# Kernel optimization log

Measured on AMD Instinct MI355X. Metric: run time of the kernel, lower is better.

## Reference

```python
import jax, jax.numpy as jnp
import numpy as np

B, L, C, D, K = 32, 36864, 16, 512, 24


def setup_inputs() -> dict:
    key = jax.random.key(0)
    ks = jax.random.split(key, 5)
    x = jax.random.normal(ks[0], (B, L, C), jnp.float32)
    # offset-conv weights scaled small so predicted offsets are O(0.2) (kaiming-ish but tame)
    w_off = jax.random.normal(ks[1], (2 * K, C, K), jnp.float32) * 0.01
    b_off = jax.random.normal(ks[2], (2 * K,), jnp.float32) * 0.05
    w_def = jax.random.normal(ks[3], (D, C, K), jnp.float32) * (2.0 / (C * K)) ** 0.5
    b_def = jax.random.normal(ks[4], (D,), jnp.float32) * 0.05
    return {"x": x, "w_off": w_off, "b_off": b_off, "w_def": w_def, "b_def": b_def}


def reference(x, w_off, b_off, w_def, b_def):
    # x: [B, L, C] -> torch view [B, C, 1, L]; H == 1 throughout.
    Bn, Ln, Cn = x.shape
    twoK, _, Kn = w_off.shape
    Lout = Ln // Kn
    xc = jnp.transpose(x, (0, 2, 1))                 # [B, C, L]
    xk = xc.reshape(Bn, Cn, Lout, Kn)                # stride == kernel -> non-overlapping windows
    # offset conv: [B, 2K, Lout]
    off = jnp.einsum('bclk,ock->bol', xk, w_off) + b_off[None, :, None]
    off = off.reshape(Bn, Kn, 2, Lout)               # channel 2k -> dy, 2k+1 -> dx (torchvision layout)
    dy = jnp.transpose(off[:, :, 0, :], (0, 2, 1))   # [B, Lout, K]
    dx = jnp.transpose(off[:, :, 1, :], (0, 2, 1))   # [B, Lout, K]
    # sampling positions along width; base = w_out*K + k
    base = jnp.arange(Lout * Kn, dtype=x.dtype).reshape(Lout, Kn)
    px = base[None] + dx                             # [B, Lout, K]
    # height bilinear weight: with H=1, contribution at h=0 is max(0, 1-|dy|)
    wy = jnp.maximum(jnp.array(0, x.dtype), 1.0 - jnp.abs(dy))
    # width bilinear with zero padding (torchvision bilinear_interpolate semantics)
    valid = (px > -1.0) & (px < Ln)
    x0 = jnp.floor(px)
    lw = px - x0                                     # weight for right neighbor
    i0 = x0.astype(jnp.int32)
    i1 = i0 + 1
    m0 = (valid & (i0 >= 0) & (i0 < Ln)).astype(x.dtype)
    m1 = (valid & (i1 >= 0) & (i1 < Ln)).astype(x.dtype)
    i0c = jnp.broadcast_to(jnp.clip(i0, 0, Ln - 1).reshape(Bn, 1, Lout * Kn), (Bn, Cn, Lout * Kn))
    i1c = jnp.broadcast_to(jnp.clip(i1, 0, Ln - 1).reshape(Bn, 1, Lout * Kn), (Bn, Cn, Lout * Kn))
    v0 = jnp.take_along_axis(xc, i0c, axis=2).reshape(Bn, Cn, Lout, Kn)
    v1 = jnp.take_along_axis(xc, i1c, axis=2).reshape(Bn, Cn, Lout, Kn)
    val = (v0 * ((1.0 - lw) * m0)[:, None] + v1 * (lw * m1)[:, None]) * wy[:, None]  # [B,C,Lout,K]
    out = jnp.einsum('bclk,dck->bld', val, w_def) + b_def  # [B, Lout, D]
    return out
```

## Files before the change

kernel.cpp:

```cpp
#include <hip/hip_runtime.h>
#include <stdint.h>

#define BATCH 32
#define LLEN  36864
#define CCH   16
#define DOUT  512
#define KW    24
#define LOUT  1536
#define MROWS (BATCH * LOUT)
#define CK    384
#define TWOK  48

typedef float fx4 __attribute__((ext_vector_type(4)));
typedef float f32x4 __attribute__((ext_vector_type(4)));
typedef __bf16 bf16x8 __attribute__((ext_vector_type(8)));
typedef uint32_t u32x4 __attribute__((ext_vector_type(4)));

__device__ __forceinline__ void gload16(void* lds, const void* g)
{
    __builtin_amdgcn_global_load_lds(
        (const __attribute__((address_space(1))) uint32_t*)g,
        (__attribute__((address_space(3))) uint32_t*)lds, 16, 0, 0);
}

__global__ __launch_bounds__(256) void prep_kernel(
    const float* __restrict__ w_off, const float* __restrict__ w_def,
    __bf16* __restrict__ woff_b, __bf16* __restrict__ wdef_b)
{
    int idx = blockIdx.x * 256 + threadIdx.x;
    if (idx < TWOK * CK) {
        int o = idx / CK, rem = idx % CK;
        int k = rem >> 4, c = rem & 15;
        woff_b[idx] = (__bf16)w_off[o * CK + c * KW + k];
    }
    if (idx < DOUT * CK) {
        int d = idx / CK, rem = idx % CK;
        int k = rem >> 4, c = rem & 15;
        wdef_b[idx] = (__bf16)w_def[d * CK + c * KW + k];
    }
}

#define BM 96
#define BN 512
#define BK 64

__global__ __launch_bounds__(512) void gemm_fused(
    const float* __restrict__ x, const __bf16* __restrict__ woff_b,
    const float* __restrict__ b_off, const __bf16* __restrict__ Bw,
    const float* __restrict__ bias, float* __restrict__ out)
{
    __shared__ __bf16 As[BM * BK];
    __shared__ char  smemB[BN * BK * 2];
    __bf16* Bs    = (__bf16*)smemB;
    __bf16* WoffS = (__bf16*)smemB;
    float*  offS  = (float*)(smemB + 38144);

    const int t = threadIdx.x;
    const int m0 = blockIdx.x * BM;
    const int wave = t >> 6, lane = t & 63;
    const int quad = lane >> 4, l16 = lane & 15;
    const int wr = wave >> 2, wc = wave & 3;

    const int mloc = t >> 2, k4 = t & 3;
    const int Mrow = m0 + mloc;
    const int b    = m0 / LOUT;
    const int lb   = Mrow - b * LOUT;
    const float* xb = x + (size_t)b * LLEN * CCH;

#pragma unroll
    for (int i = 0; i < 5; ++i) {
        int q = t + 512 * i;
        if (q < 2304) {
            int row = q / 48, cc = q - row * 48;
            *(u32x4*)&WoffS[row * 392 + cc * 8] =
                *(const u32x4*)&woff_b[row * CK + cc * 8];
        }
    }
    __syncthreads();

    if (wave < 6) {
        const float* xr = x + (size_t)(m0 + wave * 16 + l16) * CK;
        f32x4 oacc[3] = {};
#pragma unroll
        for (int ks = 0; ks < 12; ++ks) {
            int k0 = ks * 32 + quad * 8;
            fx4 a0 = *(const fx4*)&xr[k0];
            fx4 a1 = *(const fx4*)&xr[k0 + 4];
            bf16x8 af;
            af[0] = (__bf16)a0.x; af[1] = (__bf16)a0.y;
            af[2] = (__bf16)a0.z; af[3] = (__bf16)a0.w;
            af[4] = (__bf16)a1.x; af[5] = (__bf16)a1.y;
            af[6] = (__bf16)a1.z; af[7] = (__bf16)a1.w;
#pragma unroll
            for (int j = 0; j < 3; ++j) {
                bf16x8 bf = *(const bf16x8*)&WoffS[(j * 16 + l16) * 392 + k0];
                oacc[j] = __builtin_amdgcn_mfma_f32_16x16x32_bf16(af, bf, oacc[j], 0, 0, 0);
            }
        }
        float bo[3];
#pragma unroll
        for (int j = 0; j < 3; ++j) bo[j] = b_off[j * 16 + l16];
#pragma unroll
        for (int j = 0; j < 3; ++j)
#pragma unroll
            for (int r = 0; r < 4; ++r)
                offS[(wave * 16 + quad * 4 + r) * 49 + j * 16 + l16] = oacc[j][r] + bo[j];
    }
    __syncthreads();

    uint32_t dxyr[6];
    if (t < 4 * BM) {
#pragma unroll
        for (int cc = 0; cc < 6; ++cc) {
            int kk = 4 * cc + k4;
            float dy = offS[mloc * 49 + 2 * kk];
            float dx = offS[mloc * 49 + 2 * kk + 1];
            union { __bf16 h[2]; uint32_t u; } p;
            p.h[0] = (__bf16)dy; p.h[1] = (__bf16)dx;
            dxyr[cc] = p.u;
        }
    }

    f32x4 acc[3][8] = {};
    fx4 g0[4], g1[4];
    float w0, w1;

    auto load_pair = [&](uint32_t pk, int kk) {
        union { uint32_t u; __bf16 h[2]; } p; p.u = pk;
        float dy = (float)p.h[0], dx = (float)p.h[1];
        float wy  = fmaxf(0.f, 1.f - fabsf(dy));
        float px  = (float)(lb * KW + kk) + dx;
        float x0f = floorf(px);
        float lw  = px - x0f;
        int   i0  = (int)x0f;
        bool valid = (px > -1.0f) && (px < (float)LLEN);
        w0 = (valid && i0 >= 0)         ? (1.f - lw) * wy : 0.f;
        w1 = (valid && (i0 + 1) < LLEN) ? lw * wy         : 0.f;
        int i0c = min(max(i0, 0), LLEN - 1);
        int i1c = min(max(i0 + 1, 0), LLEN - 1);
        const fx4* p0 = (const fx4*)&xb[(size_t)i0c * CCH];
        const fx4* p1 = (const fx4*)&xb[(size_t)i1c * CCH];
#pragma unroll
        for (int q = 0; q < 4; ++q) { g0[q] = p0[q]; g1[q] = p1[q]; }
    };

    if (t < 4 * BM) load_pair(dxyr[0], k4);

#pragma unroll
    for (int cc = 0; cc < 6; ++cc) {
        const int kt = cc * BK;
        __syncthreads();
        if (t < 4 * BM) {
            bf16x8 oa, ob;
#pragma unroll
            for (int q = 0; q < 2; ++q) {
                fx4 v0 = g0[q], v1 = g1[q];
                oa[q * 4 + 0] = (__bf16)(w0 * v0.x + w1 * v1.x);
                oa[q * 4 + 1] = (__bf16)(w0 * v0.y + w1 * v1.y);
                oa[q * 4 + 2] = (__bf16)(w0 * v0.z + w1 * v1.z);
                oa[q * 4 + 3] = (__bf16)(w0 * v0.w + w1 * v1.w);
            }
#pragma unroll
            for (int q = 0; q < 2; ++q) {
                fx4 v0 = g0[q + 2], v1 = g1[q + 2];
                ob[q * 4 + 0] = (__bf16)(w0 * v0.x + w1 * v1.x);
                ob[q * 4 + 1] = (__bf16)(w0 * v0.y + w1 * v1.y);
                ob[q * 4 + 2] = (__bf16)(w0 * v0.z + w1 * v1.z);
                ob[q * 4 + 3] = (__bf16)(w0 * v0.w + w1 * v1.w);
            }
            int g = 2 * k4;
            *(bf16x8*)&As[mloc * BK + ((g ^ (mloc & 7)) * 8)]       = oa;
            *(bf16x8*)&As[mloc * BK + (((g + 1) ^ (mloc & 7)) * 8)] = ob;
        }
#pragma unroll
        for (int it = 0; it < 8; ++it) {
            int q = it * 512 + t;
            int r = q >> 3, c8 = q & 7;
            int sc = c8 ^ (r & 7);
            gload16(&Bs[q * 8], Bw + (size_t)r * CK + kt + sc * 8);
        }
        __syncthreads();
        if (cc + 1 < 6 && t < 4 * BM)
            load_pair(dxyr[cc + 1], 4 * (cc + 1) + k4);
#pragma unroll
        for (int ks = 0; ks < 2; ++ks) {
            bf16x8 af[3], bfr[8];
#pragma unroll
            for (int i = 0; i < 3; ++i) {
                int row = wr * 48 + i * 16 + l16;
                af[i] = *(const bf16x8*)&As[row * BK + (((ks * 4 + quad) ^ (row & 7)) * 8)];
            }
#pragma unroll
            for (int j = 0; j < 8; ++j) {
                int col = wc * 128 + j * 16 + l16;
                bfr[j] = *(const bf16x8*)&Bs[col * BK + (((ks * 4 + quad) ^ (col & 7)) * 8)];
            }
#pragma unroll
            for (int i = 0; i < 3; ++i)
#pragma unroll
                for (int j = 0; j < 8; ++j)
                    acc[i][j] = __builtin_amdgcn_mfma_f32_16x16x32_bf16(
                        af[i], bfr[j], acc[i][j], 0, 0, 0);
        }
    }

#pragma unroll
    for (int j = 0; j < 8; ++j) {
        int col = wc * 128 + j * 16 + l16;
        float bj = bias[col];
#pragma unroll
        for (int i = 0; i < 3; ++i) {
            int rowb = m0 + wr * 48 + i * 16 + quad * 4;
#pragma unroll
            for (int r = 0; r < 4; ++r)
                out[(size_t)(rowb + r) * DOUT + col] = acc[i][j][r] + bj;
        }
    }
}

extern "C" void kernel_launch(void* const* d_in, const int* in_sizes, int n_in,
                              void* d_out, int out_size, void* d_ws, size_t ws_size,
                              hipStream_t stream)
{
    const float* x     = (const float*)d_in[0];
    const float* w_off = (const float*)d_in[1];
    const float* b_off = (const float*)d_in[2];
    const float* w_def = (const float*)d_in[3];
    const float* b_def = (const float*)d_in[4];
    float* out = (float*)d_out;

    char* ws = (char*)d_ws;
    __bf16* wdef_b = (__bf16*)ws;
    __bf16* woff_b = (__bf16*)(ws + 393216);

    prep_kernel<<<768, 256, 0, stream>>>(w_off, w_def, woff_b, wdef_b);
    gemm_fused<<<MROWS / BM, 512, 0, stream>>>(x, woff_b, b_off, wdef_b, b_def, out);
}
```

Measured before the change: 196.2 us.

## Read weight fragments directly from global memory and double-buffer A tile in LDS

The B (w_def) tile is no longer staged through LDS. Each wave now loads its bf16 fragments straight from global/L2. The A tile is double-buffered, which removes one of the two barriers per K-step, and s_setprio is raised around the MFMA section. This is meant to cut LDS traffic, LDS footprint and synchronisation, at the cost of many more redundant global loads of the weights, served by cache. Each of the 4 wave-rows reads the same weights, so L2/L1 bandwidth and latency may become the bottleneck.

```diff
diff --git a/kernel.cpp b/kernel.cpp
--- a/kernel.cpp
+++ b/kernel.cpp
@@ -16,13 +16,6 @@
 typedef __bf16 bf16x8 __attribute__((ext_vector_type(8)));
 typedef uint32_t u32x4 __attribute__((ext_vector_type(4)));
 
-__device__ __forceinline__ void gload16(void* lds, const void* g)
-{
-    __builtin_amdgcn_global_load_lds(
-        (const __attribute__((address_space(1))) uint32_t*)g,
-        (__attribute__((address_space(3))) uint32_t*)lds, 16, 0, 0);
-}
-
 __global__ __launch_bounds__(256) void prep_kernel(
     const float* __restrict__ w_off, const float* __restrict__ w_def,
     __bf16* __restrict__ woff_b, __bf16* __restrict__ wdef_b)
@@ -49,11 +42,10 @@
     const float* __restrict__ b_off, const __bf16* __restrict__ Bw,
     const float* __restrict__ bias, float* __restrict__ out)
 {
-    __shared__ __bf16 As[BM * BK];
-    __shared__ char  smemB[BN * BK * 2];
-    __bf16* Bs    = (__bf16*)smemB;
-    __bf16* WoffS = (__bf16*)smemB;
-    float*  offS  = (float*)(smemB + 38144);
+    __shared__ char smem[57344];
+    __bf16* WoffS = (__bf16*)smem;
+    float*  offS  = (float*)(smem + 38144);
+    __bf16* As    = (__bf16*)smem;
 
     const int t = threadIdx.x;
     const int m0 = blockIdx.x * BM;
@@ -149,7 +141,7 @@
 #pragma unroll
     for (int cc = 0; cc < 6; ++cc) {
         const int kt = cc * BK;
-        __syncthreads();
+        __bf16* Ab = As + (cc & 1) * (BM * BK);
         if (t < 4 * BM) {
             bf16x8 oa, ob;
 #pragma unroll
@@ -169,31 +161,25 @@
                 ob[q * 4 + 3] = (__bf16)(w0 * v0.w + w1 * v1.w);
             }
             int g = 2 * k4;
-            *(bf16x8*)&As[mloc * BK + ((g ^ (mloc & 7)) * 8)]       = oa;
-            *(bf16x8*)&As[mloc * BK + (((g + 1) ^ (mloc & 7)) * 8)] = ob;
-        }
-#pragma unroll
-        for (int it = 0; it < 8; ++it) {
-            int q = it * 512 + t;
-            int r = q >> 3, c8 = q & 7;
-            int sc = c8 ^ (r & 7);
-            gload16(&Bs[q * 8], Bw + (size_t)r * CK + kt + sc * 8);
+            *(bf16x8*)&Ab[mloc * BK + ((g ^ (mloc & 7)) * 8)]       = oa;
+            *(bf16x8*)&Ab[mloc * BK + (((g + 1) ^ (mloc & 7)) * 8)] = ob;
         }
         __syncthreads();
         if (cc + 1 < 6 && t < 4 * BM)
             load_pair(dxyr[cc + 1], 4 * (cc + 1) + k4);
+        __builtin_amdgcn_s_setprio(1);
 #pragma unroll
         for (int ks = 0; ks < 2; ++ks) {
             bf16x8 af[3], bfr[8];
 #pragma unroll
             for (int i = 0; i < 3; ++i) {
                 int row = wr * 48 + i * 16 + l16;
-                af[i] = *(const bf16x8*)&As[row * BK + (((ks * 4 + quad) ^ (row & 7)) * 8)];
+                af[i] = *(const bf16x8*)&Ab[row * BK + (((ks * 4 + quad) ^ (row & 7)) * 8)];
             }
 #pragma unroll
             for (int j = 0; j < 8; ++j) {
                 int col = wc * 128 + j * 16 + l16;
-                bfr[j] = *(const bf16x8*)&Bs[col * BK + (((ks * 4 + quad) ^ (col & 7)) * 8)];
+                bfr[j] = *(const bf16x8*)&Bw[(size_t)col * CK + kt + (ks * 4 + quad) * 8];
             }
 #pragma unroll
             for (int i = 0; i < 3; ++i)
@@ -202,6 +188,7 @@
                     acc[i][j] = __builtin_amdgcn_mfma_f32_16x16x32_bf16(
                         af[i], bfr[j], acc[i][j], 0, 0, 0);
         }
+        __builtin_amdgcn_s_setprio(0);
     }
 
 #pragma unroll
```

After: 227.4 us. 15.9% more time.

## Double-buffer weight tiles in half-K phases with manual waitcnt pipelining

Applied to the files above, without the earlier changes.

Splits each 64-wide K step into two 32-wide phases and uses two LDS buffers for the weight tile. The DMA for the next phase is issued while MFMAs run on the current one, with explicit vmcnt/lgkmcnt waits, raw s_barriers, sched barriers and priority bumps around the MFMA blocks. The goal is to hide global-to-LDS load latency that the old single-buffer loop exposed behind its two __syncthreads per step. The risk is that the hand-counted vmcnt values (which differ between waves depending on how many gather loads are in flight) could be wrong, and LDS use grows to 76KB.

```diff
diff --git a/kernel.cpp b/kernel.cpp
--- a/kernel.cpp
+++ b/kernel.cpp
@@ -16,6 +16,11 @@
 typedef __bf16 bf16x8 __attribute__((ext_vector_type(8)));
 typedef uint32_t u32x4 __attribute__((ext_vector_type(4)));
 
+#define VMCNT(n)  asm volatile("s_waitcnt vmcnt(" #n ")" ::: "memory")
+#define LGKMCNT0  asm volatile("s_waitcnt lgkmcnt(0)" ::: "memory")
+#define SCHEDB    __builtin_amdgcn_sched_barrier(0)
+#define SBAR      __builtin_amdgcn_s_barrier()
+
 __device__ __forceinline__ void gload16(void* lds, const void* g)
 {
     __builtin_amdgcn_global_load_lds(
@@ -49,11 +54,12 @@
     const float* __restrict__ b_off, const __bf16* __restrict__ Bw,
     const float* __restrict__ bias, float* __restrict__ out)
 {
-    __shared__ __bf16 As[BM * BK];
-    __shared__ char  smemB[BN * BK * 2];
-    __bf16* Bs    = (__bf16*)smemB;
-    __bf16* WoffS = (__bf16*)smemB;
-    float*  offS  = (float*)(smemB + 38144);
+    __shared__ char smem[77824];
+    __bf16* As  = (__bf16*)smem;
+    __bf16* Bs0 = (__bf16*)(smem + 12288);
+    __bf16* Bs1 = (__bf16*)(smem + 45056);
+    __bf16* WoffS = (__bf16*)smem;
+    float*  offS  = (float*)(smem + 45056);
 
     const int t = threadIdx.x;
     const int m0 = blockIdx.x * BM;
@@ -144,12 +150,47 @@
         for (int q = 0; q < 4; ++q) { g0[q] = p0[q]; g1[q] = p1[q]; }
     };
 
+    auto dma_phase = [&](int ph, __bf16* buf) {
+#pragma unroll
+        for (int it = 0; it < 4; ++it) {
+            int q = it * 512 + t;
+            int c = q >> 2, s = q & 3;
+            int ss = s ^ ((c >> 1) & 3);
+            gload16(&buf[q * 8], Bw + (size_t)c * CK + ph * 32 + ss * 8);
+        }
+    };
+
+    auto mfma_phase = [&](int ks, const __bf16* Bsb) {
+        bf16x8 af[3], bfr[8];
+#pragma unroll
+        for (int i = 0; i < 3; ++i) {
+            int row = wr * 48 + i * 16 + l16;
+            af[i] = *(const bf16x8*)&As[row * BK + (((ks * 4 + quad) ^ (row & 7)) * 8)];
+        }
+#pragma unroll
+        for (int j = 0; j < 8; ++j) {
+            int col = wc * 128 + j * 16 + l16;
+            bfr[j] = *(const bf16x8*)&Bsb[col * 32 + ((quad ^ ((col >> 1) & 3)) * 8)];
+        }
+#pragma unroll
+        for (int i = 0; i < 3; ++i)
+#pragma unroll
+            for (int j = 0; j < 8; ++j)
+                acc[i][j] = __builtin_amdgcn_mfma_f32_16x16x32_bf16(
+                    af[i], bfr[j], acc[i][j], 0, 0, 0);
+    };
+
     if (t < 4 * BM) load_pair(dxyr[0], k4);
+    SCHEDB;
+    dma_phase(0, Bs0);
+    SCHEDB;
 
 #pragma unroll
     for (int cc = 0; cc < 6; ++cc) {
-        const int kt = cc * BK;
-        __syncthreads();
+        SBAR;
+        SCHEDB;
+        VMCNT(4);
+        SCHEDB;
         if (t < 4 * BM) {
             bf16x8 oa, ob;
 #pragma unroll
@@ -172,36 +213,36 @@
             *(bf16x8*)&As[mloc * BK + ((g ^ (mloc & 7)) * 8)]       = oa;
             *(bf16x8*)&As[mloc * BK + (((g + 1) ^ (mloc & 7)) * 8)] = ob;
         }
-#pragma unroll
-        for (int it = 0; it < 8; ++it) {
-            int q = it * 512 + t;
-            int r = q >> 3, c8 = q & 7;
-            int sc = c8 ^ (r & 7);
-            gload16(&Bs[q * 8], Bw + (size_t)r * CK + kt + sc * 8);
-        }
-        __syncthreads();
+        SCHEDB;
+        dma_phase(2 * cc + 1, Bs1);
+        SCHEDB;
         if (cc + 1 < 6 && t < 4 * BM)
             load_pair(dxyr[cc + 1], 4 * (cc + 1) + k4);
-#pragma unroll
-        for (int ks = 0; ks < 2; ++ks) {
-            bf16x8 af[3], bfr[8];
-#pragma unroll
-            for (int i = 0; i < 3; ++i) {
-                int row = wr * 48 + i * 16 + l16;
-                af[i] = *(const bf16x8*)&As[row * BK + (((ks * 4 + quad) ^ (row & 7)) * 8)];
-            }
-#pragma unroll
-            for (int j = 0; j < 8; ++j) {
-                int col = wc * 128 + j * 16 + l16;
-                bfr[j] = *(const bf16x8*)&Bs[col * BK + (((ks * 4 + quad) ^ (col & 7)) * 8)];
-            }
-#pragma unroll
-            for (int i = 0; i < 3; ++i)
-#pragma unroll
-                for (int j = 0; j < 8; ++j)
-                    acc[i][j] = __builtin_amdgcn_mfma_f32_16x16x32_bf16(
-                        af[i], bfr[j], acc[i][j], 0, 0, 0);
-        }
+        SCHEDB;
+        LGKMCNT0;
+        SCHEDB;
+        SBAR;
+        SCHEDB;
+        if (cc < 5) { if (wave < 6) { VMCNT(12); } else { VMCNT(4); } }
+        else        { VMCNT(4); }
+        SCHEDB;
+        SBAR;
+        SCHEDB;
+        __builtin_amdgcn_s_setprio(1);
+        mfma_phase(0, Bs0);
+        __builtin_amdgcn_s_setprio(0);
+        SCHEDB;
+        if (cc < 5) { if (wave < 6) { VMCNT(8); } else { VMCNT(0); } }
+        else        { VMCNT(0); }
+        SCHEDB;
+        SBAR;
+        SCHEDB;
+        if (cc < 5) dma_phase(2 * cc + 2, Bs0);
+        SCHEDB;
+        __builtin_amdgcn_s_setprio(1);
+        mfma_phase(1, Bs1);
+        __builtin_amdgcn_s_setprio(0);
+        SCHEDB;
     }
 
 #pragma unroll
```

Result: no change. 194.4 us (-0.9%).
